# Optimization experiments

Measured on AMD Instinct MI355X. Metric: run time of the kernel, lower is better.

The kernel has to match this reference:

```python
import jax, jax.numpy as jnp
import numpy as np

N, P, H = 4096, 128, 4
E = P // H           # per-head embed dim (=32)
NSEG = 32            # number of distinct position segments
NEG = -1e30          # mask fill (safe finite -inf)


def setup_inputs() -> dict:
    key = jax.random.key(0)
    ks = jax.random.split(key, 8)
    s = 1.0 / np.sqrt(P)
    return {
        "inp": jax.random.normal(ks[0], (N, P), jnp.float32),
        "pos": jax.random.randint(ks[1], (N,), 0, NSEG, jnp.int32),
        "Wq": jax.random.normal(ks[2], (P, P), jnp.float32) * s,
        "bq": jnp.zeros((P,), jnp.float32),
        "Wk": jax.random.normal(ks[3], (P, P), jnp.float32) * s,
        "bk": jnp.zeros((P,), jnp.float32),
        "Wv": jax.random.normal(ks[4], (P, P), jnp.float32) * s,
        "bv": jnp.zeros((P,), jnp.float32),
    }


def reference(inp, pos, Wq, bq, Wk, bk, Wv, bv):
    # Per-segment multi-head self-attention. The TF while_loop gathers rows of
    # each unique `pos` value, runs attention within that segment, and scatters
    # results back to the original row order. This is mathematically identical
    # to full attention with a same-segment mask (softmax restricted to keys
    # in the same segment), which is the vectorized form here.
    n = inp.shape[0]

    def heads(x, W, b):
        # (n, p) -> (h, n, e), matching rearrange 'n (h e) -> h n e'
        y = x @ W + b
        return y.reshape(n, H, E).transpose(1, 0, 2)

    q = heads(inp, Wq, bq)
    k = heads(inp, Wk, bk)
    v = heads(inp, Wv, bv)

    score = jnp.einsum('hne,hme->hnm', q, k) / np.sqrt(E).astype(np.float32)
    same_seg = (pos[:, None] == pos[None, :])[None, :, :]      # (1, n, n)
    score = jnp.where(same_seg, score, NEG)
    weight = jax.nn.softmax(score, axis=-1)                    # (h, n, n)
    out = jnp.einsum('hnm,hme->hne', weight, v)                # (h, n, e)
    # rearrange 'h n e -> n (h e)'
    return out.transpose(1, 0, 2).reshape(n, P)
```

## Files before the change

kernel.cpp:

```cpp
#include <hip/hip_runtime.h>
#include <hip/hip_bf16.h>
#include <math.h>

#define N 4096
#define P 128
#define H 4
#define E 32
#define NSEG 32
#define TPB 256
#define PROJ_TASKS 192

#define LENMAX 256
#define VSTRIDE 264
#define NEGF -3.0e38f

typedef __attribute__((ext_vector_type(8))) short bf16x8;
typedef __attribute__((ext_vector_type(4))) float f32x4;
typedef unsigned short u16;

__device__ __forceinline__ u16 f2b(float x) {
    __hip_bfloat16 b = __float2bfloat16(x);
    return *(u16*)&b;
}

__device__ __forceinline__ void sort_phase(const int* __restrict__ pos,
                                           int* __restrict__ seg_rows,
                                           int* __restrict__ seg_off,
                                           int* sm, int t) {
    int* cnt = sm;
    int* cur = sm + NSEG;
    int* off = sm + 2 * NSEG;
    if (t < NSEG) cnt[t] = 0;
    __syncthreads();
    for (int i = t; i < N; i += TPB) atomicAdd(&cnt[pos[i]], 1);
    __syncthreads();
    if (t == 0) {
        int s = 0;
        for (int k = 0; k < NSEG; ++k) { off[k] = s; s += cnt[k]; }
        off[NSEG] = s;
    }
    __syncthreads();
    if (t <= NSEG) seg_off[t] = off[t];
    if (t < NSEG) cur[t] = off[t];
    __syncthreads();
    for (int i = t; i < N; i += TPB) {
        int r = atomicAdd(&cur[pos[i]], 1);
        seg_rows[r] = i;
    }
}

__device__ __forceinline__ void proj_phase(int task,
                                           const float* __restrict__ x,
                                           const float* __restrict__ Wq, const float* __restrict__ bq,
                                           const float* __restrict__ Wk, const float* __restrict__ bk,
                                           const float* __restrict__ Wv, const float* __restrict__ bv,
                                           u16* __restrict__ Q, u16* __restrict__ Ko, u16* __restrict__ Vo,
                                           float* sm, int t) {
    float* Xl = sm;
    float* Wl = sm + 8192;

    const int mat = task >> 6;
    const int r0  = (task & 63) * 64;
    const float* W = (mat == 0) ? Wq : (mat == 1) ? Wk : Wv;
    const float* b = (mat == 0) ? bq : (mat == 1) ? bk : bv;
    u16* y         = (mat == 0) ? Q  : (mat == 1) ? Ko : Vo;

    for (int i = t * 4; i < 64 * 128; i += TPB * 4) {
        *(float4*)(Xl + i) = *(const float4*)(x + (size_t)r0 * 128 + i);
    }

    const int tc = t & 31;
    const int tr = t >> 5;

    float4 bb = *(const float4*)(b + tc * 4);
    float4 acc[8];
#pragma unroll
    for (int r = 0; r < 8; ++r) acc[r] = bb;

    for (int kc = 0; kc < 128; kc += 32) {
        __syncthreads();
        for (int i = t * 4; i < 32 * 128; i += TPB * 4) {
            *(float4*)(Wl + i) = *(const float4*)(W + (size_t)kc * 128 + i);
        }
        __syncthreads();
#pragma unroll
        for (int k0 = 0; k0 < 32; k0 += 4) {
            float4 w0 = *(float4*)&Wl[(k0 + 0) * 128 + tc * 4];
            float4 w1 = *(float4*)&Wl[(k0 + 1) * 128 + tc * 4];
            float4 w2 = *(float4*)&Wl[(k0 + 2) * 128 + tc * 4];
            float4 w3 = *(float4*)&Wl[(k0 + 3) * 128 + tc * 4];
#pragma unroll
            for (int r = 0; r < 8; ++r) {
                float4 xv = *(float4*)&Xl[(tr * 8 + r) * 128 + kc + k0];
                acc[r].x = fmaf(xv.x, w0.x, acc[r].x);
                acc[r].y = fmaf(xv.x, w0.y, acc[r].y);
                acc[r].z = fmaf(xv.x, w0.z, acc[r].z);
                acc[r].w = fmaf(xv.x, w0.w, acc[r].w);
                acc[r].x = fmaf(xv.y, w1.x, acc[r].x);
                acc[r].y = fmaf(xv.y, w1.y, acc[r].y);
                acc[r].z = fmaf(xv.y, w1.z, acc[r].z);
                acc[r].w = fmaf(xv.y, w1.w, acc[r].w);
                acc[r].x = fmaf(xv.z, w2.x, acc[r].x);
                acc[r].y = fmaf(xv.z, w2.y, acc[r].y);
                acc[r].z = fmaf(xv.z, w2.z, acc[r].z);
                acc[r].w = fmaf(xv.z, w2.w, acc[r].w);
                acc[r].x = fmaf(xv.w, w3.x, acc[r].x);
                acc[r].y = fmaf(xv.w, w3.y, acc[r].y);
                acc[r].z = fmaf(xv.w, w3.z, acc[r].z);
                acc[r].w = fmaf(xv.w, w3.w, acc[r].w);
            }
        }
    }

#pragma unroll
    for (int r = 0; r < 8; ++r) {
        ushort4 st;
        st.x = f2b(acc[r].x); st.y = f2b(acc[r].y);
        st.z = f2b(acc[r].z); st.w = f2b(acc[r].w);
        *(ushort4*)(y + (size_t)(r0 + tr * 8 + r) * 128 + tc * 4) = st;
    }
}

__global__ __launch_bounds__(TPB) void sort_proj_kernel(
        const float* __restrict__ inp, const int* __restrict__ pos,
        const float* __restrict__ Wq, const float* __restrict__ bq,
        const float* __restrict__ Wk, const float* __restrict__ bk,
        const float* __restrict__ Wv, const float* __restrict__ bv,
        u16* __restrict__ Q, u16* __restrict__ Kb, u16* __restrict__ Vb,
        int* __restrict__ seg_rows, int* __restrict__ seg_off) {
    __shared__ __align__(16) float sm[12288];
    const int b = blockIdx.x;
    const int t = threadIdx.x;
    if (b == 0) {
        sort_phase(pos, seg_rows, seg_off, (int*)sm, t);
    } else {
        proj_phase(b - 1, inp, Wq, bq, Wk, bk, Wv, bv, Q, Kb, Vb, sm, t);
    }
}

__device__ __forceinline__ void tile_qk(int tt, int beg, int len, int h,
                                        const u16* __restrict__ Qb,
                                        const u16* __restrict__ Kb,
                                        const int* __restrict__ seg_rows,
                                        u16* __restrict__ Ps,
                                        int col, int quad, float* lrow) {
    const float scale = 0.17677669529663687f;
    const int qi = beg + min(tt * 16 + col, len - 1);
    const bf16x8 qa = *(const bf16x8*)(Qb + (size_t)seg_rows[qi] * 128 + h * 32 + quad * 8);

    int krow[16];
#pragma unroll
    for (int kt = 0; kt < 16; ++kt)
        krow[kt] = seg_rows[beg + min(kt * 16 + col, len - 1)];

    f32x4 S[16];
#pragma unroll
    for (int kt = 0; kt < 16; ++kt) {
        const bf16x8 kb = *(const bf16x8*)(Kb + (size_t)krow[kt] * 128 + h * 32 + quad * 8);
        f32x4 c = {0.f, 0.f, 0.f, 0.f};
        S[kt] = __builtin_amdgcn_mfma_f32_16x16x32_bf16(qa, kb, c, 0, 0, 0);
    }

    float mrow[4] = {NEGF, NEGF, NEGF, NEGF};
#pragma unroll
    for (int kt = 0; kt < 16; ++kt) {
        const bool kvalid = (kt * 16 + col) < len;
#pragma unroll
        for (int r = 0; r < 4; ++r) {
            const float sc = kvalid ? S[kt][r] * scale : NEGF;
            S[kt][r] = sc;
            mrow[r] = fmaxf(mrow[r], sc);
        }
    }
#pragma unroll
    for (int d = 1; d < 16; d <<= 1) {
#pragma unroll
        for (int r = 0; r < 4; ++r)
            mrow[r] = fmaxf(mrow[r], __shfl_xor(mrow[r], d));
    }
    lrow[0] = lrow[1] = lrow[2] = lrow[3] = 0.f;
#pragma unroll
    for (int kt = 0; kt < 16; ++kt) {
#pragma unroll
        for (int r = 0; r < 4; ++r) {
            const float p = __expf(S[kt][r] - mrow[r]);
            S[kt][r] = p;
            lrow[r] += p;
        }
    }
#pragma unroll
    for (int d = 1; d < 16; d <<= 1) {
#pragma unroll
        for (int r = 0; r < 4; ++r)
            lrow[r] += __shfl_xor(lrow[r], d);
    }
#pragma unroll
    for (int kt = 0; kt < 16; ++kt) {
#pragma unroll
        for (int r = 0; r < 4; ++r)
            Ps[(quad * 4 + r) * VSTRIDE + kt * 16 + col] = f2b(S[kt][r]);
    }
}

__device__ __forceinline__ void tile_pv(int tt, int beg, int len, int h,
                                        const u16* __restrict__ Vt,
                                        const u16* __restrict__ Ps,
                                        const int* __restrict__ seg_rows,
                                        float* __restrict__ out,
                                        int col, int quad, const float* lrow) {
    f32x4 o0 = {0.f, 0.f, 0.f, 0.f}, o1 = {0.f, 0.f, 0.f, 0.f};
#pragma unroll
    for (int kg = 0; kg < 8; ++kg) {
        const bf16x8 pa = *(const bf16x8*)(Ps + col * VSTRIDE + kg * 32 + quad * 8);
        const bf16x8 v0 = *(const bf16x8*)(Vt + col * VSTRIDE + kg * 32 + quad * 8);
        const bf16x8 v1 = *(const bf16x8*)(Vt + (16 + col) * VSTRIDE + kg * 32 + quad * 8);
        o0 = __builtin_amdgcn_mfma_f32_16x16x32_bf16(pa, v0, o0, 0, 0, 0);
        o1 = __builtin_amdgcn_mfma_f32_16x16x32_bf16(pa, v1, o1, 0, 0, 0);
    }
#pragma unroll
    for (int r = 0; r < 4; ++r) {
        const int qloc = tt * 16 + quad * 4 + r;
        if (qloc < len) {
            const float inv = 1.0f / lrow[r];
            float* op = out + (size_t)seg_rows[beg + qloc] * 128 + h * 32;
            op[col]      = o0[r] * inv;
            op[16 + col] = o1[r] * inv;
        }
    }
}

__global__ __launch_bounds__(TPB) void attn_kernel(const u16* __restrict__ Qb,
                                                   const u16* __restrict__ Kb,
                                                   const u16* __restrict__ Vb,
                                                   const int* __restrict__ seg_rows,
                                                   const int* __restrict__ seg_off,
                                                   float* __restrict__ out) {
    __shared__ u16 smu[VSTRIDE * (32 + 4 * 16)];

    const int s = blockIdx.x, h = blockIdx.y, z = blockIdx.z;
    const int beg = seg_off[s];
    const int len = seg_off[s + 1] - beg;
    if (z * 64 >= len) return;
    const int t = threadIdx.x, w = t >> 6;
    const int lane = t & 63, col = lane & 15, quad = lane >> 4;

    u16* Vt = smu;
#pragma unroll
    for (int ii = 0; ii < 4; ++ii) {
        const int idx = ii * TPB + t;
        const int key = idx >> 2, c = idx & 3;
        bf16x8 v = {0, 0, 0, 0, 0, 0, 0, 0};
        if (key < len)
            v = *(const bf16x8*)(Vb + (size_t)seg_rows[beg + key] * 128 + h * 32 + c * 8);
#pragma unroll
        for (int j = 0; j < 8; ++j)
            Vt[(c * 8 + j) * VSTRIDE + key] = (u16)v[j];
    }

    u16* Ps = smu + (32 + w * 16) * VSTRIDE;

    const int tt0 = z * 4 + w;
    const bool have0 = (tt0 * 16 < len);
    float lr0[4];
    if (have0)
        tile_qk(tt0, beg, len, h, Qb, Kb, seg_rows, Ps, col, quad, lr0);

    __syncthreads();

    if (have0)
        tile_pv(tt0, beg, len, h, Vt, Ps, seg_rows, out, col, quad, lr0);

    for (int tt = tt0 + 8; tt * 16 < len; tt += 8) {
        float lr[4];
        tile_qk(tt, beg, len, h, Qb, Kb, seg_rows, Ps, col, quad, lr);
        tile_pv(tt, beg, len, h, Vt, Ps, seg_rows, out, col, quad, lr);
    }
}

extern "C" void kernel_launch(void* const* d_in, const int* in_sizes, int n_in,
                              void* d_out, int out_size, void* d_ws, size_t ws_size,
                              hipStream_t stream) {
    const float* inp = (const float*)d_in[0];
    const int*   pos = (const int*)d_in[1];
    const float* Wq  = (const float*)d_in[2];
    const float* bq  = (const float*)d_in[3];
    const float* Wk  = (const float*)d_in[4];
    const float* bk  = (const float*)d_in[5];
    const float* Wv  = (const float*)d_in[6];
    const float* bv  = (const float*)d_in[7];
    float* out = (float*)d_out;

    u16* Qb = (u16*)d_ws;
    u16* Kb = Qb + (size_t)N * 128;
    u16* Vb = Kb + (size_t)N * 128;
    int* seg_rows = (int*)(Vb + (size_t)N * 128);
    int* seg_off  = seg_rows + N;

    sort_proj_kernel<<<1 + PROJ_TASKS, TPB, 0, stream>>>(
        inp, pos, Wq, bq, Wk, bk, Wv, bv, Qb, Kb, Vb, seg_rows, seg_off);

    attn_kernel<<<dim3(NSEG, H, 2), TPB, 0, stream>>>(
        Qb, Kb, Vb, seg_rows, seg_off, out);
}
```

Before: 92.49 us.

## Scatter projected Q/K/V into segment-sorted order to make attention loads contiguous

The sort now also writes an inverse permutation. The projection kernel uses it to store Q, K and V rows directly in segment-sorted order, so the attention kernel reads them contiguously instead of gathering through seg_rows. To do this, sort and projection are split into two separate launches, which adds a launch and a serialization: projection can no longer overlap with the single-block sort. Attention loads become coalesced and the index indirection is removed from the inner QK loop.

```diff
diff --git a/kernel.cpp b/kernel.cpp
--- a/kernel.cpp
+++ b/kernel.cpp
@@ -23,13 +23,14 @@
     return *(u16*)&b;
 }
 
-__device__ __forceinline__ void sort_phase(const int* __restrict__ pos,
-                                           int* __restrict__ seg_rows,
-                                           int* __restrict__ seg_off,
-                                           int* sm, int t) {
-    int* cnt = sm;
-    int* cur = sm + NSEG;
-    int* off = sm + 2 * NSEG;
+__global__ __launch_bounds__(TPB) void sort_kernel(const int* __restrict__ pos,
+                                                   int* __restrict__ seg_rows,
+                                                   int* __restrict__ seg_off,
+                                                   int* __restrict__ perm) {
+    __shared__ int cnt[NSEG];
+    __shared__ int cur[NSEG];
+    __shared__ int off[NSEG + 1];
+    const int t = threadIdx.x;
     if (t < NSEG) cnt[t] = 0;
     __syncthreads();
     for (int i = t; i < N; i += TPB) atomicAdd(&cnt[pos[i]], 1);
@@ -44,26 +45,30 @@
     if (t < NSEG) cur[t] = off[t];
     __syncthreads();
     for (int i = t; i < N; i += TPB) {
-        int r = atomicAdd(&cur[pos[i]], 1);
+        const int r = atomicAdd(&cur[pos[i]], 1);
         seg_rows[r] = i;
-    }
-}
-
-__device__ __forceinline__ void proj_phase(int task,
-                                           const float* __restrict__ x,
-                                           const float* __restrict__ Wq, const float* __restrict__ bq,
-                                           const float* __restrict__ Wk, const float* __restrict__ bk,
-                                           const float* __restrict__ Wv, const float* __restrict__ bv,
-                                           u16* __restrict__ Q, u16* __restrict__ Ko, u16* __restrict__ Vo,
-                                           float* sm, int t) {
+        perm[i] = r;
+    }
+}
+
+__global__ __launch_bounds__(TPB) void proj_kernel(
+        const float* __restrict__ x,
+        const float* __restrict__ Wq, const float* __restrict__ bq,
+        const float* __restrict__ Wk, const float* __restrict__ bk,
+        const float* __restrict__ Wv, const float* __restrict__ bv,
+        const int* __restrict__ perm,
+        u16* __restrict__ Qs, u16* __restrict__ Ks, u16* __restrict__ Vs) {
+    __shared__ __align__(16) float sm[12288];
     float* Xl = sm;
     float* Wl = sm + 8192;
 
+    const int task = blockIdx.x;
+    const int t = threadIdx.x;
     const int mat = task >> 6;
     const int r0  = (task & 63) * 64;
     const float* W = (mat == 0) ? Wq : (mat == 1) ? Wk : Wv;
     const float* b = (mat == 0) ? bq : (mat == 1) ? bk : bv;
-    u16* y         = (mat == 0) ? Q  : (mat == 1) ? Ko : Vo;
+    u16* y         = (mat == 0) ? Qs : (mat == 1) ? Ks : Vs;
 
     for (int i = t * 4; i < 64 * 128; i += TPB * 4) {
         *(float4*)(Xl + i) = *(const float4*)(x + (size_t)r0 * 128 + i);
@@ -114,49 +119,28 @@
 
 #pragma unroll
     for (int r = 0; r < 8; ++r) {
+        const int dst = perm[r0 + tr * 8 + r];
         ushort4 st;
         st.x = f2b(acc[r].x); st.y = f2b(acc[r].y);
         st.z = f2b(acc[r].z); st.w = f2b(acc[r].w);
-        *(ushort4*)(y + (size_t)(r0 + tr * 8 + r) * 128 + tc * 4) = st;
-    }
-}
-
-__global__ __launch_bounds__(TPB) void sort_proj_kernel(
-        const float* __restrict__ inp, const int* __restrict__ pos,
-        const float* __restrict__ Wq, const float* __restrict__ bq,
-        const float* __restrict__ Wk, const float* __restrict__ bk,
-        const float* __restrict__ Wv, const float* __restrict__ bv,
-        u16* __restrict__ Q, u16* __restrict__ Kb, u16* __restrict__ Vb,
-        int* __restrict__ seg_rows, int* __restrict__ seg_off) {
-    __shared__ __align__(16) float sm[12288];
-    const int b = blockIdx.x;
-    const int t = threadIdx.x;
-    if (b == 0) {
-        sort_phase(pos, seg_rows, seg_off, (int*)sm, t);
-    } else {
-        proj_phase(b - 1, inp, Wq, bq, Wk, bk, Wv, bv, Q, Kb, Vb, sm, t);
+        *(ushort4*)(y + (size_t)dst * 128 + tc * 4) = st;
     }
 }
 
 __device__ __forceinline__ void tile_qk(int tt, int beg, int len, int h,
-                                        const u16* __restrict__ Qb,
-                                        const u16* __restrict__ Kb,
-                                        const int* __restrict__ seg_rows,
+                                        const u16* __restrict__ Qs,
+                                        const u16* __restrict__ Ks,
                                         u16* __restrict__ Ps,
                                         int col, int quad, float* lrow) {
     const float scale = 0.17677669529663687f;
-    const int qi = beg + min(tt * 16 + col, len - 1);
-    const bf16x8 qa = *(const bf16x8*)(Qb + (size_t)seg_rows[qi] * 128 + h * 32 + quad * 8);
-
-    int krow[16];
-#pragma unroll
-    for (int kt = 0; kt < 16; ++kt)
-        krow[kt] = seg_rows[beg + min(kt * 16 + col, len - 1)];
+    const int qrow = beg + min(tt * 16 + col, len - 1);
+    const bf16x8 qa = *(const bf16x8*)(Qs + (size_t)qrow * 128 + h * 32 + quad * 8);
 
     f32x4 S[16];
 #pragma unroll
     for (int kt = 0; kt < 16; ++kt) {
-        const bf16x8 kb = *(const bf16x8*)(Kb + (size_t)krow[kt] * 128 + h * 32 + quad * 8);
+        const int krow = beg + min(kt * 16 + col, len - 1);
+        const bf16x8 kb = *(const bf16x8*)(Ks + (size_t)krow * 128 + h * 32 + quad * 8);
         f32x4 c = {0.f, 0.f, 0.f, 0.f};
         S[kt] = __builtin_amdgcn_mfma_f32_16x16x32_bf16(qa, kb, c, 0, 0, 0);
     }
@@ -221,17 +205,18 @@
     for (int r = 0; r < 4; ++r) {
         const int qloc = tt * 16 + quad * 4 + r;
         if (qloc < len) {
+            const int orow = seg_rows[beg + qloc];
             const float inv = 1.0f / lrow[r];
-            float* op = out + (size_t)seg_rows[beg + qloc] * 128 + h * 32;
+            float* op = out + (size_t)orow * 128 + h * 32;
             op[col]      = o0[r] * inv;
             op[16 + col] = o1[r] * inv;
         }
     }
 }
 
-__global__ __launch_bounds__(TPB) void attn_kernel(const u16* __restrict__ Qb,
-                                                   const u16* __restrict__ Kb,
-                                                   const u16* __restrict__ Vb,
+__global__ __launch_bounds__(TPB) void attn_kernel(const u16* __restrict__ Qs,
+                                                   const u16* __restrict__ Ks,
+                                                   const u16* __restrict__ Vs,
                                                    const int* __restrict__ seg_rows,
                                                    const int* __restrict__ seg_off,
                                                    float* __restrict__ out) {
@@ -251,7 +236,7 @@
         const int key = idx >> 2, c = idx & 3;
         bf16x8 v = {0, 0, 0, 0, 0, 0, 0, 0};
         if (key < len)
-            v = *(const bf16x8*)(Vb + (size_t)seg_rows[beg + key] * 128 + h * 32 + c * 8);
+            v = *(const bf16x8*)(Vs + (size_t)(beg + key) * 128 + h * 32 + c * 8);
 #pragma unroll
         for (int j = 0; j < 8; ++j)
             Vt[(c * 8 + j) * VSTRIDE + key] = (u16)v[j];
@@ -263,7 +248,7 @@
     const bool have0 = (tt0 * 16 < len);
     float lr0[4];
     if (have0)
-        tile_qk(tt0, beg, len, h, Qb, Kb, seg_rows, Ps, col, quad, lr0);
+        tile_qk(tt0, beg, len, h, Qs, Ks, Ps, col, quad, lr0);
 
     __syncthreads();
 
@@ -272,7 +257,7 @@
 
     for (int tt = tt0 + 8; tt * 16 < len; tt += 8) {
         float lr[4];
-        tile_qk(tt, beg, len, h, Qb, Kb, seg_rows, Ps, col, quad, lr);
+        tile_qk(tt, beg, len, h, Qs, Ks, Ps, col, quad, lr);
         tile_pv(tt, beg, len, h, Vt, Ps, seg_rows, out, col, quad, lr);
     }
 }
@@ -290,15 +275,18 @@
     const float* bv  = (const float*)d_in[7];
     float* out = (float*)d_out;
 
-    u16* Qb = (u16*)d_ws;
-    u16* Kb = Qb + (size_t)N * 128;
-    u16* Vb = Kb + (size_t)N * 128;
-    int* seg_rows = (int*)(Vb + (size_t)N * 128);
+    u16* Qs = (u16*)d_ws;
+    u16* Ks = Qs + (size_t)N * 128;
+    u16* Vs = Ks + (size_t)N * 128;
+    int* seg_rows = (int*)(Vs + (size_t)N * 128);
     int* seg_off  = seg_rows + N;
-
-    sort_proj_kernel<<<1 + PROJ_TASKS, TPB, 0, stream>>>(
-        inp, pos, Wq, bq, Wk, bk, Wv, bv, Qb, Kb, Vb, seg_rows, seg_off);
+    int* perm     = seg_off + NSEG + 1;
+
+    sort_kernel<<<1, TPB, 0, stream>>>(pos, seg_rows, seg_off, perm);
+
+    proj_kernel<<<PROJ_TASKS, TPB, 0, stream>>>(
+        inp, Wq, bq, Wk, bk, Wv, bv, perm, Qs, Ks, Vs);
 
     attn_kernel<<<dim3(NSEG, H, 2), TPB, 0, stream>>>(
-        Qb, Kb, Vb, seg_rows, seg_off, out);
-}
+        Qs, Ks, Vs, seg_rows, seg_off, out);
+}
```

New measurement: 101.9 us. +10.2%, slower.
